# Optimization experiments

Measured on AMD Instinct MI355X. Metric: run time of the kernel, lower is better.

The kernel has to match this reference:

```python
import jax, jax.numpy as jnp
import numpy as np

N_NODES = 8192
N_EDGES = 524288
D_IN = 256
D_OUT = 256


def setup_inputs() -> dict:
    key = jax.random.key(0)
    ks = jax.random.split(key, 8)
    h = jax.random.normal(ks[0], (N_NODES, D_IN), dtype=jnp.float32)
    # Xavier-uniform-like scale for weights
    s = (6.0 / (D_IN + D_OUT)) ** 0.5
    W = jax.random.uniform(ks[1], (D_IN, D_OUT), jnp.float32, -s, s)
    Wq = jax.random.uniform(ks[2], (D_IN, D_OUT), jnp.float32, -s, s)
    bq = jnp.zeros((D_OUT,), jnp.float32)
    Wk = jax.random.uniform(ks[3], (D_IN, D_OUT), jnp.float32, -s, s)
    bk = jnp.zeros((D_OUT,), jnp.float32)
    senders = jax.random.randint(ks[4], (N_EDGES,), 0, N_NODES, dtype=jnp.int64 if jax.config.jax_enable_x64 else jnp.int32)
    receivers = jax.random.randint(ks[5], (N_EDGES,), 0, N_NODES, dtype=jnp.int64 if jax.config.jax_enable_x64 else jnp.int32)
    return {"h": h, "W": W, "Wq": Wq, "bq": bq, "Wk": Wk, "bk": bk,
            "senders": senders, "receivers": receivers}


def reference(h, W, Wq, bq, Wk, bk, senders, receivers):
    # Projected node features: (N, D_OUT)
    h_proj = jnp.dot(h, W)
    # Dense attention logits a = q @ k^T: (N, N), as in the original module
    q = jnp.dot(h, Wq) + bq
    k = jnp.dot(h, Wk) + bk
    a = jnp.dot(q, k.T)
    # Gather per-edge messages and attention weights, weight, scatter-add
    messages = h_proj[senders] * a[senders, receivers][:, None]  # (E, D_OUT)
    aggregated = jax.ops.segment_sum(messages, receivers, num_segments=h.shape[0])
    return jax.nn.relu(aggregated)
```

## Files before the change

kernel.cpp:

```cpp
#include <hip/hip_runtime.h>
#include <stdint.h>

typedef unsigned short u16;
typedef unsigned int u32;
typedef short v8s __attribute__((ext_vector_type(8)));
typedef float v4f __attribute__((ext_vector_type(4)));

#define N_NODES 8192
#define N_EDGES 524288
#define DFEAT 256
#define PADC 160

static __device__ __forceinline__ float bflo(u32 u) { return __uint_as_float(u << 16); }
static __device__ __forceinline__ float bfhi(u32 u) { return __uint_as_float(u & 0xffff0000u); }
static __device__ __forceinline__ u16 f2bf(float f) {
    u32 u = __float_as_uint(f);
    return (u16)((u + 0x7fffu + ((u >> 16) & 1u)) >> 16);
}

__global__ void prep_small(const float* __restrict__ w0, const float* __restrict__ w1,
                           const float* __restrict__ w2, u16* __restrict__ wt,
                           int* __restrict__ cnt) {
    int b = blockIdx.x;
    if (b < 48) {
        __shared__ u16 t[64][65];
        int region = b >> 4, tile = b & 15;
        int k0 = (tile >> 2) * 64, n0 = (tile & 3) * 64;
        const float* w = (region == 0) ? w0 : ((region == 1) ? w1 : w2);
        int tx = threadIdx.x & 63, ty = threadIdx.x >> 6;
#pragma unroll
        for (int it = 0; it < 16; it++) {
            int row = it * 4 + ty;
            t[row][tx] = f2bf(w[(k0 + row) * 256 + n0 + tx]);
        }
        __syncthreads();
        u16* o = wt + region * 65536;
#pragma unroll
        for (int it = 0; it < 16; it++) {
            int row = it * 4 + ty;
            o[(n0 + row) * 256 + k0 + tx] = t[tx][row];
        }
    } else {
        int i = ((b - 48) * 256 + threadIdx.x) * 4;
        *(int4*)(cnt + i) = make_int4(0, 0, 0, 0);
    }
}

__global__ __launch_bounds__(256) void main_mid(
    const float* __restrict__ h, const u16* __restrict__ wt,
    const float* __restrict__ bq, const float* __restrict__ bk,
    const int* __restrict__ recv, const int* __restrict__ send,
    u16* __restrict__ hproj, u16* __restrict__ qbuf, u16* __restrict__ kbuf,
    int* __restrict__ cnt, u16* __restrict__ es) {
    int b = blockIdx.x;
    if (b < 2048) {
        int e = b * 256 + threadIdx.x;
        int r = recv[e];
        int s = send[e];
        int pos = atomicAdd(&cnt[r], 1);
        if (pos < PADC) es[r * PADC + pos] = (u16)s;
    } else {
        int g = b - 2048;
        int wave = threadIdx.x >> 6, lane = threadIdx.x & 63;
        int lm = lane & 15, lq = lane >> 4;
        int bx = g & 127, by = g >> 7;
        int m0 = bx * 64 + wave * 16;
        int region = by >> 2, n0b = (by & 3) * 64;
        const u16* wtr = wt + region * 65536;

        v4f acc[4];
#pragma unroll
        for (int nt = 0; nt < 4; nt++) acc[nt] = (v4f){0.f, 0.f, 0.f, 0.f};

        const float* arow = h + (m0 + lm) * 256 + lq * 8;
#pragma unroll
        for (int k0 = 0; k0 < 256; k0 += 32) {
            float4 f0 = *(const float4*)(arow + k0);
            float4 f1 = *(const float4*)(arow + k0 + 4);
            v8s a;
            a[0] = (short)f2bf(f0.x); a[1] = (short)f2bf(f0.y);
            a[2] = (short)f2bf(f0.z); a[3] = (short)f2bf(f0.w);
            a[4] = (short)f2bf(f1.x); a[5] = (short)f2bf(f1.y);
            a[6] = (short)f2bf(f1.z); a[7] = (short)f2bf(f1.w);
#pragma unroll
            for (int nt = 0; nt < 4; nt++) {
                v8s bb = *(const v8s*)(wtr + (n0b + nt * 16 + lm) * 256 + k0 + lq * 8);
                acc[nt] = __builtin_amdgcn_mfma_f32_16x16x32_bf16(a, bb, acc[nt], 0, 0, 0);
            }
        }
        u16* outp = (region == 0) ? hproj : ((region == 1) ? qbuf : kbuf);
        const float* bias = (region == 1) ? bq : ((region == 2) ? bk : nullptr);
#pragma unroll
        for (int nt = 0; nt < 4; nt++) {
            int nn = n0b + nt * 16 + lm;
            float bv = bias ? bias[nn] : 0.f;
#pragma unroll
            for (int i = 0; i < 4; i++) {
                int m = m0 + lq * 4 + i;
                outp[m * 256 + nn] = f2bf(acc[nt][i] + bv);
            }
        }
    }
}


#define DOT8(Q) (kr0 * bflo((Q).x) + kr1 * bfhi((Q).x)                        \
               + kr2 * bflo((Q).y) + kr3 * bfhi((Q).y)                        \
               + kr4 * bflo((Q).z) + kr5 * bfhi((Q).z)                        \
               + kr6 * bflo((Q).w) + kr7 * bfhi((Q).w))

#define AXPY(P, H) do {                                                       \
    a0 += (P) * bflo((H).x); a1 += (P) * bfhi((H).x);                         \
    a2 += (P) * bflo((H).y); a3 += (P) * bfhi((H).y);                         \
    a4 += (P) * bflo((H).z); a5 += (P) * bfhi((H).z);                         \
    a6 += (P) * bflo((H).w); a7 += (P) * bfhi((H).w);                         \
} while (0)

#define DOT_AGG1(SIDX) do {                                                   \
    int off_ = (int)(SIDX) * 256 + cb;                                        \
    uint4 qv_ = *(const uint4*)(qbuf + off_);                                 \
    uint4 hv_ = *(const uint4*)(hpb + off_);                                  \
    float p_ = DOT8(qv_);                                                     \
    p_ += __shfl_xor(p_, 1, 32);  p_ += __shfl_xor(p_, 2, 32);                \
    p_ += __shfl_xor(p_, 4, 32);  p_ += __shfl_xor(p_, 8, 32);                \
    p_ += __shfl_xor(p_, 16, 32);                                             \
    AXPY(p_, hv_);                                                            \
} while (0)

__global__ __launch_bounds__(256, 4) void edge_fused(
    const u16* __restrict__ qbuf, const u16* __restrict__ kbuf,
    const u16* __restrict__ hpb, const int* __restrict__ cnt,
    const u16* __restrict__ es, float* __restrict__ out) {
    int wave = threadIdx.x >> 6, lane = threadIdx.x & 63;
    int r = blockIdx.x * 4 + wave;
    int lh = lane & 31, half = lane >> 5;
    int cb = lh * 8;
    int n = min(cnt[r], PADC);
    int base = r * PADC;

    uint4 kv = *(const uint4*)(kbuf + r * 256 + cb);
    float kr0 = bflo(kv.x), kr1 = bfhi(kv.x), kr2 = bflo(kv.y), kr3 = bfhi(kv.y),
          kr4 = bflo(kv.z), kr5 = bfhi(kv.z), kr6 = bflo(kv.w), kr7 = bfhi(kv.w);

    float a0 = 0.f, a1 = 0.f, a2 = 0.f, a3 = 0.f,
          a4 = 0.f, a5 = 0.f, a6 = 0.f, a7 = 0.f;

    uint2 sp = *(const uint2*)(es + base + half * 4);
    for (int c0 = 0; c0 < n; c0 += 8) {
        int nx = c0 + 8;
        uint2 spn = sp;
        if (nx < n) spn = *(const uint2*)(es + base + nx + half * 4);

        if (nx <= n) {
            int s0 = (int)(sp.x & 0xffffu), s1 = (int)(sp.x >> 16);
            int s2 = (int)(sp.y & 0xffffu), s3 = (int)(sp.y >> 16);
            int o0 = s0 * 256 + cb, o1 = s1 * 256 + cb;
            int o2 = s2 * 256 + cb, o3 = s3 * 256 + cb;
            uint4 q0 = *(const uint4*)(qbuf + o0);
            uint4 q1 = *(const uint4*)(qbuf + o1);
            uint4 q2 = *(const uint4*)(qbuf + o2);
            uint4 q3 = *(const uint4*)(qbuf + o3);
            uint4 h0 = *(const uint4*)(hpb + o0);
            uint4 h1 = *(const uint4*)(hpb + o1);
            uint4 h2 = *(const uint4*)(hpb + o2);
            uint4 h3 = *(const uint4*)(hpb + o3);
            float p0 = DOT8(q0);
            float p1 = DOT8(q1);
            float p2 = DOT8(q2);
            float p3 = DOT8(q3);
            p0 += __shfl_xor(p0, 1, 32);  p1 += __shfl_xor(p1, 1, 32);
            p2 += __shfl_xor(p2, 1, 32);  p3 += __shfl_xor(p3, 1, 32);
            p0 += __shfl_xor(p0, 2, 32);  p1 += __shfl_xor(p1, 2, 32);
            p2 += __shfl_xor(p2, 2, 32);  p3 += __shfl_xor(p3, 2, 32);
            p0 += __shfl_xor(p0, 4, 32);  p1 += __shfl_xor(p1, 4, 32);
            p2 += __shfl_xor(p2, 4, 32);  p3 += __shfl_xor(p3, 4, 32);
            p0 += __shfl_xor(p0, 8, 32);  p1 += __shfl_xor(p1, 8, 32);
            p2 += __shfl_xor(p2, 8, 32);  p3 += __shfl_xor(p3, 8, 32);
            p0 += __shfl_xor(p0, 16, 32); p1 += __shfl_xor(p1, 16, 32);
            p2 += __shfl_xor(p2, 16, 32); p3 += __shfl_xor(p3, 16, 32);
            AXPY(p0, h0);
            AXPY(p1, h1);
            AXPY(p2, h2);
            AXPY(p3, h3);
        } else {
            int mrem = n - c0 - half * 4;
            if (mrem > 0) DOT_AGG1(sp.x & 0xffffu);
            if (mrem > 1) DOT_AGG1(sp.x >> 16);
            if (mrem > 2) DOT_AGG1(sp.y & 0xffffu);
            if (mrem > 3) DOT_AGG1(sp.y >> 16);
        }
        sp = spn;
    }

    a0 += __shfl_xor(a0, 32, 64); a1 += __shfl_xor(a1, 32, 64);
    a2 += __shfl_xor(a2, 32, 64); a3 += __shfl_xor(a3, 32, 64);
    a4 += __shfl_xor(a4, 32, 64); a5 += __shfl_xor(a5, 32, 64);
    a6 += __shfl_xor(a6, 32, 64); a7 += __shfl_xor(a7, 32, 64);

    if (half == 0) {
        float4 o0, o1;
        o0.x = fmaxf(a0, 0.f); o0.y = fmaxf(a1, 0.f);
        o0.z = fmaxf(a2, 0.f); o0.w = fmaxf(a3, 0.f);
        o1.x = fmaxf(a4, 0.f); o1.y = fmaxf(a5, 0.f);
        o1.z = fmaxf(a6, 0.f); o1.w = fmaxf(a7, 0.f);
        float* op = out + r * 256 + cb;
        *(float4*)op = o0;
        *(float4*)(op + 4) = o1;
    }
}

extern "C" void kernel_launch(void* const* d_in, const int* in_sizes, int n_in,
                              void* d_out, int out_size, void* d_ws, size_t ws_size,
                              hipStream_t stream) {
    const float* h  = (const float*)d_in[0];
    const float* W  = (const float*)d_in[1];
    const float* Wq = (const float*)d_in[2];
    const float* bq = (const float*)d_in[3];
    const float* Wk = (const float*)d_in[4];
    const float* bk = (const float*)d_in[5];
    const int* senders   = (const int*)d_in[6];
    const int* receivers = (const int*)d_in[7];
    float* out = (float*)d_out;

    char* ws = (char*)d_ws;
    u16* wt    = (u16*)ws;
    u16* hproj = (u16*)(ws + 393216);
    u16* qbuf  = hproj + N_NODES * DFEAT;
    u16* kbuf  = qbuf + N_NODES * DFEAT;
    int* cnt   = (int*)(kbuf + N_NODES * DFEAT);
    u16* es    = (u16*)(cnt + N_NODES);

    prep_small<<<56, 256, 0, stream>>>(W, Wq, Wk, wt, cnt);
    main_mid<<<3584, 256, 0, stream>>>(h, wt, bq, bk, receivers, senders,
                                       hproj, qbuf, kbuf, cnt, es);
    edge_fused<<<N_NODES / 4, 256, 0, stream>>>(qbuf, kbuf, hproj, cnt, es, out);
}
```

Before: 182.2 us.

## Fuse all stages into one cooperative persistent kernel with grid syncs

Merges the weight transpose, edge bucketing, projection GEMMs and the edge aggregation into a single cooperative kernel. Grid-wide syncs separate the phases and blocks loop persistently over the work items, which removes two kernel launches and their gaps. It also pads the per-receiver counters to a 16-int stride to spread atomic contention, and widens the aggregation loop to 8 edges per half-wave for more loads in flight. In exchange it adds grid.sync costs and caps occupancy at what a cooperative launch can keep resident. The larger unrolled loop also raises register pressure.

```diff
diff --git a/kernel.cpp b/kernel.cpp
--- a/kernel.cpp
+++ b/kernel.cpp
@@ -1,5 +1,8 @@
 #include <hip/hip_runtime.h>
+#include <hip/hip_cooperative_groups.h>
 #include <stdint.h>
+
+namespace cg = cooperative_groups;
 
 typedef unsigned short u16;
 typedef unsigned int u32;
@@ -10,6 +13,7 @@
 #define N_EDGES 524288
 #define DFEAT 256
 #define PADC 160
+#define CNTS 16
 
 static __device__ __forceinline__ float bflo(u32 u) { return __uint_as_float(u << 16); }
 static __device__ __forceinline__ float bfhi(u32 u) { return __uint_as_float(u & 0xffff0000u); }
@@ -17,92 +21,6 @@
     u32 u = __float_as_uint(f);
     return (u16)((u + 0x7fffu + ((u >> 16) & 1u)) >> 16);
 }
-
-__global__ void prep_small(const float* __restrict__ w0, const float* __restrict__ w1,
-                           const float* __restrict__ w2, u16* __restrict__ wt,
-                           int* __restrict__ cnt) {
-    int b = blockIdx.x;
-    if (b < 48) {
-        __shared__ u16 t[64][65];
-        int region = b >> 4, tile = b & 15;
-        int k0 = (tile >> 2) * 64, n0 = (tile & 3) * 64;
-        const float* w = (region == 0) ? w0 : ((region == 1) ? w1 : w2);
-        int tx = threadIdx.x & 63, ty = threadIdx.x >> 6;
-#pragma unroll
-        for (int it = 0; it < 16; it++) {
-            int row = it * 4 + ty;
-            t[row][tx] = f2bf(w[(k0 + row) * 256 + n0 + tx]);
-        }
-        __syncthreads();
-        u16* o = wt + region * 65536;
-#pragma unroll
-        for (int it = 0; it < 16; it++) {
-            int row = it * 4 + ty;
-            o[(n0 + row) * 256 + k0 + tx] = t[tx][row];
-        }
-    } else {
-        int i = ((b - 48) * 256 + threadIdx.x) * 4;
-        *(int4*)(cnt + i) = make_int4(0, 0, 0, 0);
-    }
-}
-
-__global__ __launch_bounds__(256) void main_mid(
-    const float* __restrict__ h, const u16* __restrict__ wt,
-    const float* __restrict__ bq, const float* __restrict__ bk,
-    const int* __restrict__ recv, const int* __restrict__ send,
-    u16* __restrict__ hproj, u16* __restrict__ qbuf, u16* __restrict__ kbuf,
-    int* __restrict__ cnt, u16* __restrict__ es) {
-    int b = blockIdx.x;
-    if (b < 2048) {
-        int e = b * 256 + threadIdx.x;
-        int r = recv[e];
-        int s = send[e];
-        int pos = atomicAdd(&cnt[r], 1);
-        if (pos < PADC) es[r * PADC + pos] = (u16)s;
-    } else {
-        int g = b - 2048;
-        int wave = threadIdx.x >> 6, lane = threadIdx.x & 63;
-        int lm = lane & 15, lq = lane >> 4;
-        int bx = g & 127, by = g >> 7;
-        int m0 = bx * 64 + wave * 16;
-        int region = by >> 2, n0b = (by & 3) * 64;
-        const u16* wtr = wt + region * 65536;
-
-        v4f acc[4];
-#pragma unroll
-        for (int nt = 0; nt < 4; nt++) acc[nt] = (v4f){0.f, 0.f, 0.f, 0.f};
-
-        const float* arow = h + (m0 + lm) * 256 + lq * 8;
-#pragma unroll
-        for (int k0 = 0; k0 < 256; k0 += 32) {
-            float4 f0 = *(const float4*)(arow + k0);
-            float4 f1 = *(const float4*)(arow + k0 + 4);
-            v8s a;
-            a[0] = (short)f2bf(f0.x); a[1] = (short)f2bf(f0.y);
-            a[2] = (short)f2bf(f0.z); a[3] = (short)f2bf(f0.w);
-            a[4] = (short)f2bf(f1.x); a[5] = (short)f2bf(f1.y);
-            a[6] = (short)f2bf(f1.z); a[7] = (short)f2bf(f1.w);
-#pragma unroll
-            for (int nt = 0; nt < 4; nt++) {
-                v8s bb = *(const v8s*)(wtr + (n0b + nt * 16 + lm) * 256 + k0 + lq * 8);
-                acc[nt] = __builtin_amdgcn_mfma_f32_16x16x32_bf16(a, bb, acc[nt], 0, 0, 0);
-            }
-        }
-        u16* outp = (region == 0) ? hproj : ((region == 1) ? qbuf : kbuf);
-        const float* bias = (region == 1) ? bq : ((region == 2) ? bk : nullptr);
-#pragma unroll
-        for (int nt = 0; nt < 4; nt++) {
-            int nn = n0b + nt * 16 + lm;
-            float bv = bias ? bias[nn] : 0.f;
-#pragma unroll
-            for (int i = 0; i < 4; i++) {
-                int m = m0 + lq * 4 + i;
-                outp[m * 256 + nn] = f2bf(acc[nt][i] + bv);
-            }
-        }
-    }
-}
-
 
 #define DOT8(Q) (kr0 * bflo((Q).x) + kr1 * bfhi((Q).x)                        \
                + kr2 * bflo((Q).y) + kr3 * bfhi((Q).y)                        \
@@ -127,85 +45,182 @@
     AXPY(p_, hv_);                                                            \
 } while (0)
 
-__global__ __launch_bounds__(256, 4) void edge_fused(
-    const u16* __restrict__ qbuf, const u16* __restrict__ kbuf,
-    const u16* __restrict__ hpb, const int* __restrict__ cnt,
-    const u16* __restrict__ es, float* __restrict__ out) {
-    int wave = threadIdx.x >> 6, lane = threadIdx.x & 63;
-    int r = blockIdx.x * 4 + wave;
-    int lh = lane & 31, half = lane >> 5;
-    int cb = lh * 8;
-    int n = min(cnt[r], PADC);
-    int base = r * PADC;
-
-    uint4 kv = *(const uint4*)(kbuf + r * 256 + cb);
-    float kr0 = bflo(kv.x), kr1 = bfhi(kv.x), kr2 = bflo(kv.y), kr3 = bfhi(kv.y),
-          kr4 = bflo(kv.z), kr5 = bfhi(kv.z), kr6 = bflo(kv.w), kr7 = bfhi(kv.w);
-
-    float a0 = 0.f, a1 = 0.f, a2 = 0.f, a3 = 0.f,
-          a4 = 0.f, a5 = 0.f, a6 = 0.f, a7 = 0.f;
-
-    uint2 sp = *(const uint2*)(es + base + half * 4);
-    for (int c0 = 0; c0 < n; c0 += 8) {
-        int nx = c0 + 8;
-        uint2 spn = sp;
-        if (nx < n) spn = *(const uint2*)(es + base + nx + half * 4);
-
-        if (nx <= n) {
-            int s0 = (int)(sp.x & 0xffffu), s1 = (int)(sp.x >> 16);
-            int s2 = (int)(sp.y & 0xffffu), s3 = (int)(sp.y >> 16);
-            int o0 = s0 * 256 + cb, o1 = s1 * 256 + cb;
-            int o2 = s2 * 256 + cb, o3 = s3 * 256 + cb;
-            uint4 q0 = *(const uint4*)(qbuf + o0);
-            uint4 q1 = *(const uint4*)(qbuf + o1);
-            uint4 q2 = *(const uint4*)(qbuf + o2);
-            uint4 q3 = *(const uint4*)(qbuf + o3);
-            uint4 h0 = *(const uint4*)(hpb + o0);
-            uint4 h1 = *(const uint4*)(hpb + o1);
-            uint4 h2 = *(const uint4*)(hpb + o2);
-            uint4 h3 = *(const uint4*)(hpb + o3);
-            float p0 = DOT8(q0);
-            float p1 = DOT8(q1);
-            float p2 = DOT8(q2);
-            float p3 = DOT8(q3);
-            p0 += __shfl_xor(p0, 1, 32);  p1 += __shfl_xor(p1, 1, 32);
-            p2 += __shfl_xor(p2, 1, 32);  p3 += __shfl_xor(p3, 1, 32);
-            p0 += __shfl_xor(p0, 2, 32);  p1 += __shfl_xor(p1, 2, 32);
-            p2 += __shfl_xor(p2, 2, 32);  p3 += __shfl_xor(p3, 2, 32);
-            p0 += __shfl_xor(p0, 4, 32);  p1 += __shfl_xor(p1, 4, 32);
-            p2 += __shfl_xor(p2, 4, 32);  p3 += __shfl_xor(p3, 4, 32);
-            p0 += __shfl_xor(p0, 8, 32);  p1 += __shfl_xor(p1, 8, 32);
-            p2 += __shfl_xor(p2, 8, 32);  p3 += __shfl_xor(p3, 8, 32);
-            p0 += __shfl_xor(p0, 16, 32); p1 += __shfl_xor(p1, 16, 32);
-            p2 += __shfl_xor(p2, 16, 32); p3 += __shfl_xor(p3, 16, 32);
-            AXPY(p0, h0);
-            AXPY(p1, h1);
-            AXPY(p2, h2);
-            AXPY(p3, h3);
-        } else {
-            int mrem = n - c0 - half * 4;
-            if (mrem > 0) DOT_AGG1(sp.x & 0xffffu);
-            if (mrem > 1) DOT_AGG1(sp.x >> 16);
-            if (mrem > 2) DOT_AGG1(sp.y & 0xffffu);
-            if (mrem > 3) DOT_AGG1(sp.y >> 16);
-        }
-        sp = spn;
-    }
-
-    a0 += __shfl_xor(a0, 32, 64); a1 += __shfl_xor(a1, 32, 64);
-    a2 += __shfl_xor(a2, 32, 64); a3 += __shfl_xor(a3, 32, 64);
-    a4 += __shfl_xor(a4, 32, 64); a5 += __shfl_xor(a5, 32, 64);
-    a6 += __shfl_xor(a6, 32, 64); a7 += __shfl_xor(a7, 32, 64);
-
-    if (half == 0) {
-        float4 o0, o1;
-        o0.x = fmaxf(a0, 0.f); o0.y = fmaxf(a1, 0.f);
-        o0.z = fmaxf(a2, 0.f); o0.w = fmaxf(a3, 0.f);
-        o1.x = fmaxf(a4, 0.f); o1.y = fmaxf(a5, 0.f);
-        o1.z = fmaxf(a6, 0.f); o1.w = fmaxf(a7, 0.f);
-        float* op = out + r * 256 + cb;
-        *(float4*)op = o0;
-        *(float4*)(op + 4) = o1;
+#define LOADP(I, SIDX)                                                        \
+    int o##I = (int)(SIDX) * 256 + cb;                                        \
+    uint4 q##I = *(const uint4*)(qbuf + o##I);                                \
+    uint4 h##I = *(const uint4*)(hpb + o##I);
+
+__global__ __launch_bounds__(256, 4) void fused(
+    const float* __restrict__ h, const float* __restrict__ w0,
+    const float* __restrict__ w1, const float* __restrict__ w2,
+    const float* __restrict__ bq, const float* __restrict__ bk,
+    const int* __restrict__ recv, const int* __restrict__ send,
+    u16* __restrict__ wt, u16* __restrict__ hproj, u16* __restrict__ qbuf,
+    u16* __restrict__ kbuf, int* __restrict__ cnt, u16* __restrict__ es,
+    float* __restrict__ out)
+{
+    cg::grid_group grid = cg::this_grid();
+    const int nb = gridDim.x;
+    const int b = blockIdx.x;
+    const int tid = threadIdx.x;
+    const int wave = tid >> 6, lane = tid & 63;
+    __shared__ u16 t[64][65];
+
+    for (int i = b * 256 + tid; i < N_NODES * CNTS; i += nb * 256) cnt[i] = 0;
+
+    for (int j = b; j < 48; j += nb) {
+        int region = j >> 4, tile = j & 15;
+        int k0 = (tile >> 2) * 64, n0 = (tile & 3) * 64;
+        const float* w = (region == 0) ? w0 : ((region == 1) ? w1 : w2);
+        int tx = tid & 63, ty = tid >> 6;
+#pragma unroll
+        for (int it = 0; it < 16; it++) {
+            int row = it * 4 + ty;
+            t[row][tx] = f2bf(w[(k0 + row) * 256 + n0 + tx]);
+        }
+        __syncthreads();
+        u16* o = wt + region * 65536;
+#pragma unroll
+        for (int it = 0; it < 16; it++) {
+            int row = it * 4 + ty;
+            o[(n0 + row) * 256 + k0 + tx] = t[tx][row];
+        }
+        __syncthreads();
+    }
+
+    grid.sync();
+
+    for (int e = b * 256 + tid; e < N_EDGES; e += nb * 256) {
+        int r = recv[e];
+        int s = send[e];
+        int pos = atomicAdd(&cnt[r * CNTS], 1);
+        if (pos < PADC) es[r * PADC + pos] = (u16)s;
+    }
+
+    for (int j = b; j < 1536; j += nb) {
+        int lm = lane & 15, lq = lane >> 4;
+        int bx = j & 127, by = j >> 7;
+        int m0 = bx * 64 + wave * 16;
+        int region = by >> 2, n0b = (by & 3) * 64;
+        const u16* wtr = wt + region * 65536;
+
+        v4f acc[4];
+#pragma unroll
+        for (int nt = 0; nt < 4; nt++) acc[nt] = (v4f){0.f, 0.f, 0.f, 0.f};
+
+        const float* arow = h + (m0 + lm) * 256 + lq * 8;
+#pragma unroll
+        for (int k0 = 0; k0 < 256; k0 += 32) {
+            float4 f0 = *(const float4*)(arow + k0);
+            float4 f1 = *(const float4*)(arow + k0 + 4);
+            v8s a;
+            a[0] = (short)f2bf(f0.x); a[1] = (short)f2bf(f0.y);
+            a[2] = (short)f2bf(f0.z); a[3] = (short)f2bf(f0.w);
+            a[4] = (short)f2bf(f1.x); a[5] = (short)f2bf(f1.y);
+            a[6] = (short)f2bf(f1.z); a[7] = (short)f2bf(f1.w);
+#pragma unroll
+            for (int nt = 0; nt < 4; nt++) {
+                v8s bb = *(const v8s*)(wtr + (n0b + nt * 16 + lm) * 256 + k0 + lq * 8);
+                acc[nt] = __builtin_amdgcn_mfma_f32_16x16x32_bf16(a, bb, acc[nt], 0, 0, 0);
+            }
+        }
+        u16* outp = (region == 0) ? hproj : ((region == 1) ? qbuf : kbuf);
+        const float* bias = (region == 1) ? bq : ((region == 2) ? bk : nullptr);
+#pragma unroll
+        for (int nt = 0; nt < 4; nt++) {
+            int nn = n0b + nt * 16 + lm;
+            float bv = bias ? bias[nn] : 0.f;
+#pragma unroll
+            for (int i = 0; i < 4; i++) {
+                int m = m0 + lq * 4 + i;
+                outp[m * 256 + nn] = f2bf(acc[nt][i] + bv);
+            }
+        }
+    }
+
+    grid.sync();
+
+    const u16* hpb = hproj;
+    {
+        int lh = lane & 31, half = lane >> 5;
+        int cb = lh * 8;
+        for (int g = b; g < 2048; g += nb) {
+            int r = g * 4 + wave;
+            int n = min(cnt[r * CNTS], PADC);
+            int base = r * PADC;
+
+            uint4 kv = *(const uint4*)(kbuf + r * 256 + cb);
+            float kr0 = bflo(kv.x), kr1 = bfhi(kv.x), kr2 = bflo(kv.y), kr3 = bfhi(kv.y),
+                  kr4 = bflo(kv.z), kr5 = bfhi(kv.z), kr6 = bflo(kv.w), kr7 = bfhi(kv.w);
+
+            float a0 = 0.f, a1 = 0.f, a2 = 0.f, a3 = 0.f,
+                  a4 = 0.f, a5 = 0.f, a6 = 0.f, a7 = 0.f;
+
+            uint4 sp = *(const uint4*)(es + base + half * 8);
+            for (int c0 = 0; c0 < n; c0 += 16) {
+                int nx = c0 + 16;
+                uint4 spn = sp;
+                if (nx < n) spn = *(const uint4*)(es + base + nx + half * 8);
+
+                if (nx <= n) {
+                    LOADP(0, sp.x & 0xffffu) LOADP(1, sp.x >> 16)
+                    LOADP(2, sp.y & 0xffffu) LOADP(3, sp.y >> 16)
+                    LOADP(4, sp.z & 0xffffu) LOADP(5, sp.z >> 16)
+                    LOADP(6, sp.w & 0xffffu) LOADP(7, sp.w >> 16)
+                    float p0 = DOT8(q0), p1 = DOT8(q1), p2 = DOT8(q2), p3 = DOT8(q3);
+                    float p4 = DOT8(q4), p5 = DOT8(q5), p6 = DOT8(q6), p7 = DOT8(q7);
+                    p0 += __shfl_xor(p0, 1, 32);  p1 += __shfl_xor(p1, 1, 32);
+                    p2 += __shfl_xor(p2, 1, 32);  p3 += __shfl_xor(p3, 1, 32);
+                    p4 += __shfl_xor(p4, 1, 32);  p5 += __shfl_xor(p5, 1, 32);
+                    p6 += __shfl_xor(p6, 1, 32);  p7 += __shfl_xor(p7, 1, 32);
+                    p0 += __shfl_xor(p0, 2, 32);  p1 += __shfl_xor(p1, 2, 32);
+                    p2 += __shfl_xor(p2, 2, 32);  p3 += __shfl_xor(p3, 2, 32);
+                    p4 += __shfl_xor(p4, 2, 32);  p5 += __shfl_xor(p5, 2, 32);
+                    p6 += __shfl_xor(p6, 2, 32);  p7 += __shfl_xor(p7, 2, 32);
+                    p0 += __shfl_xor(p0, 4, 32);  p1 += __shfl_xor(p1, 4, 32);
+                    p2 += __shfl_xor(p2, 4, 32);  p3 += __shfl_xor(p3, 4, 32);
+                    p4 += __shfl_xor(p4, 4, 32);  p5 += __shfl_xor(p5, 4, 32);
+                    p6 += __shfl_xor(p6, 4, 32);  p7 += __shfl_xor(p7, 4, 32);
+                    p0 += __shfl_xor(p0, 8, 32);  p1 += __shfl_xor(p1, 8, 32);
+                    p2 += __shfl_xor(p2, 8, 32);  p3 += __shfl_xor(p3, 8, 32);
+                    p4 += __shfl_xor(p4, 8, 32);  p5 += __shfl_xor(p5, 8, 32);
+                    p6 += __shfl_xor(p6, 8, 32);  p7 += __shfl_xor(p7, 8, 32);
+                    p0 += __shfl_xor(p0, 16, 32); p1 += __shfl_xor(p1, 16, 32);
+                    p2 += __shfl_xor(p2, 16, 32); p3 += __shfl_xor(p3, 16, 32);
+                    p4 += __shfl_xor(p4, 16, 32); p5 += __shfl_xor(p5, 16, 32);
+                    p6 += __shfl_xor(p6, 16, 32); p7 += __shfl_xor(p7, 16, 32);
+                    AXPY(p0, h0); AXPY(p1, h1); AXPY(p2, h2); AXPY(p3, h3);
+                    AXPY(p4, h4); AXPY(p5, h5); AXPY(p6, h6); AXPY(p7, h7);
+                } else {
+                    int mrem = n - c0 - half * 8;
+                    if (mrem > 0) DOT_AGG1(sp.x & 0xffffu);
+                    if (mrem > 1) DOT_AGG1(sp.x >> 16);
+                    if (mrem > 2) DOT_AGG1(sp.y & 0xffffu);
+                    if (mrem > 3) DOT_AGG1(sp.y >> 16);
+                    if (mrem > 4) DOT_AGG1(sp.z & 0xffffu);
+                    if (mrem > 5) DOT_AGG1(sp.z >> 16);
+                    if (mrem > 6) DOT_AGG1(sp.w & 0xffffu);
+                    if (mrem > 7) DOT_AGG1(sp.w >> 16);
+                }
+                sp = spn;
+            }
+
+            a0 += __shfl_xor(a0, 32, 64); a1 += __shfl_xor(a1, 32, 64);
+            a2 += __shfl_xor(a2, 32, 64); a3 += __shfl_xor(a3, 32, 64);
+            a4 += __shfl_xor(a4, 32, 64); a5 += __shfl_xor(a5, 32, 64);
+            a6 += __shfl_xor(a6, 32, 64); a7 += __shfl_xor(a7, 32, 64);
+
+            if (half == 0) {
+                float4 o0, o1;
+                o0.x = fmaxf(a0, 0.f); o0.y = fmaxf(a1, 0.f);
+                o0.z = fmaxf(a2, 0.f); o0.w = fmaxf(a3, 0.f);
+                o1.x = fmaxf(a4, 0.f); o1.y = fmaxf(a5, 0.f);
+                o1.z = fmaxf(a6, 0.f); o1.w = fmaxf(a7, 0.f);
+                float* op = out + r * 256 + cb;
+                *(float4*)op = o0;
+                *(float4*)(op + 4) = o1;
+            }
+        }
     }
 }
 
@@ -228,10 +243,22 @@
     u16* qbuf  = hproj + N_NODES * DFEAT;
     u16* kbuf  = qbuf + N_NODES * DFEAT;
     int* cnt   = (int*)(kbuf + N_NODES * DFEAT);
-    u16* es    = (u16*)(cnt + N_NODES);
-
-    prep_small<<<56, 256, 0, stream>>>(W, Wq, Wk, wt, cnt);
-    main_mid<<<3584, 256, 0, stream>>>(h, wt, bq, bk, receivers, senders,
-                                       hproj, qbuf, kbuf, cnt, es);
-    edge_fused<<<N_NODES / 4, 256, 0, stream>>>(qbuf, kbuf, hproj, cnt, es, out);
+    u16* es    = (u16*)(cnt + N_NODES * CNTS);
+
+    static int nblk = 0;
+    if (nblk == 0) {
+        int bpc = 0;
+        if (hipOccupancyMaxActiveBlocksPerMultiprocessor(&bpc, fused, 256, 0) != hipSuccess
+            || bpc <= 0) bpc = 3;
+        nblk = bpc * 256;
+        if (nblk > 2048) nblk = 2048;
+    }
+
+    void* args[] = {
+        (void*)&h, (void*)&W, (void*)&Wq, (void*)&Wk, (void*)&bq, (void*)&bk,
+        (void*)&receivers, (void*)&senders,
+        (void*)&wt, (void*)&hproj, (void*)&qbuf, (void*)&kbuf,
+        (void*)&cnt, (void*)&es, (void*)&out
+    };
+    hipLaunchCooperativeKernel((void*)fused, dim3(nblk), dim3(256), args, 0, stream);
 }
```

New measurement: 312.6 us. +71.6%, slower.

## Software-pipeline edge gathers with double buffering and pad per-node counters

Applied to the files above, without the earlier changes.

The edge aggregation loop becomes a two-stage software pipeline. The next group of q/hproj rows is gathered while the dot products and AXPYs of the current group run, and the tail is handled once after the loop. Separately, each per-node atomic counter is padded to a 64-byte stride (CNTS=16) to cut contention and false sharing between neighbouring counters, which enlarges the zeroing launch in prep_small. The double buffering raises register pressure under the launch bound of 4 blocks, and the padded counters use more workspace.

```diff
diff --git a/kernel.cpp b/kernel.cpp
--- a/kernel.cpp
+++ b/kernel.cpp
@@ -10,6 +10,7 @@
 #define N_EDGES 524288
 #define DFEAT 256
 #define PADC 160
+#define CNTS 16
 
 static __device__ __forceinline__ float bflo(u32 u) { return __uint_as_float(u << 16); }
 static __device__ __forceinline__ float bfhi(u32 u) { return __uint_as_float(u & 0xffff0000u); }
@@ -57,7 +58,7 @@
         int e = b * 256 + threadIdx.x;
         int r = recv[e];
         int s = send[e];
-        int pos = atomicAdd(&cnt[r], 1);
+        int pos = atomicAdd(&cnt[r * CNTS], 1);
         if (pos < PADC) es[r * PADC + pos] = (u16)s;
     } else {
         int g = b - 2048;
@@ -127,6 +128,45 @@
     AXPY(p_, hv_);                                                            \
 } while (0)
 
+#define LOAD4(P, SP) do {                                                     \
+    int s0_ = (int)((SP).x & 0xffffu), s1_ = (int)((SP).x >> 16);             \
+    int s2_ = (int)((SP).y & 0xffffu), s3_ = (int)((SP).y >> 16);             \
+    q##P##0 = *(const uint4*)(qbuf + s0_ * 256 + cb);                         \
+    h##P##0 = *(const uint4*)(hpb  + s0_ * 256 + cb);                         \
+    q##P##1 = *(const uint4*)(qbuf + s1_ * 256 + cb);                         \
+    h##P##1 = *(const uint4*)(hpb  + s1_ * 256 + cb);                         \
+    q##P##2 = *(const uint4*)(qbuf + s2_ * 256 + cb);                         \
+    h##P##2 = *(const uint4*)(hpb  + s2_ * 256 + cb);                         \
+    q##P##3 = *(const uint4*)(qbuf + s3_ * 256 + cb);                         \
+    h##P##3 = *(const uint4*)(hpb  + s3_ * 256 + cb);                         \
+} while (0)
+
+#define COMP4(P) do {                                                         \
+    float p0_ = DOT8(q##P##0), p1_ = DOT8(q##P##1);                           \
+    float p2_ = DOT8(q##P##2), p3_ = DOT8(q##P##3);                           \
+    p0_ += __shfl_xor(p0_, 1, 32);  p1_ += __shfl_xor(p1_, 1, 32);            \
+    p2_ += __shfl_xor(p2_, 1, 32);  p3_ += __shfl_xor(p3_, 1, 32);            \
+    p0_ += __shfl_xor(p0_, 2, 32);  p1_ += __shfl_xor(p1_, 2, 32);            \
+    p2_ += __shfl_xor(p2_, 2, 32);  p3_ += __shfl_xor(p3_, 2, 32);            \
+    p0_ += __shfl_xor(p0_, 4, 32);  p1_ += __shfl_xor(p1_, 4, 32);            \
+    p2_ += __shfl_xor(p2_, 4, 32);  p3_ += __shfl_xor(p3_, 4, 32);            \
+    p0_ += __shfl_xor(p0_, 8, 32);  p1_ += __shfl_xor(p1_, 8, 32);            \
+    p2_ += __shfl_xor(p2_, 8, 32);  p3_ += __shfl_xor(p3_, 8, 32);            \
+    p0_ += __shfl_xor(p0_, 16, 32); p1_ += __shfl_xor(p1_, 16, 32);           \
+    p2_ += __shfl_xor(p2_, 16, 32); p3_ += __shfl_xor(p3_, 16, 32);           \
+    AXPY(p0_, h##P##0); AXPY(p1_, h##P##1);                                   \
+    AXPY(p2_, h##P##2); AXPY(p3_, h##P##3);                                   \
+} while (0)
+
+#define STAGE(CUR, NXT, TC) do {                                              \
+    if ((TC) + 1 < NT) {                                                      \
+        LOAD4(NXT, spn);                                                      \
+        if ((TC) + 2 < NT)                                                    \
+            spn = *(const uint2*)(es + base + ((TC) + 2) * 8 + half * 4);     \
+    }                                                                         \
+    COMP4(CUR);                                                               \
+} while (0)
+
 __global__ __launch_bounds__(256, 4) void edge_fused(
     const u16* __restrict__ qbuf, const u16* __restrict__ kbuf,
     const u16* __restrict__ hpb, const int* __restrict__ cnt,
@@ -135,7 +175,7 @@
     int r = blockIdx.x * 4 + wave;
     int lh = lane & 31, half = lane >> 5;
     int cb = lh * 8;
-    int n = min(cnt[r], PADC);
+    int n = min(cnt[r * CNTS], PADC);
     int base = r * PADC;
 
     uint4 kv = *(const uint4*)(kbuf + r * 256 + cb);
@@ -145,51 +185,28 @@
     float a0 = 0.f, a1 = 0.f, a2 = 0.f, a3 = 0.f,
           a4 = 0.f, a5 = 0.f, a6 = 0.f, a7 = 0.f;
 
-    uint2 sp = *(const uint2*)(es + base + half * 4);
-    for (int c0 = 0; c0 < n; c0 += 8) {
-        int nx = c0 + 8;
-        uint2 spn = sp;
-        if (nx < n) spn = *(const uint2*)(es + base + nx + half * 4);
-
-        if (nx <= n) {
-            int s0 = (int)(sp.x & 0xffffu), s1 = (int)(sp.x >> 16);
-            int s2 = (int)(sp.y & 0xffffu), s3 = (int)(sp.y >> 16);
-            int o0 = s0 * 256 + cb, o1 = s1 * 256 + cb;
-            int o2 = s2 * 256 + cb, o3 = s3 * 256 + cb;
-            uint4 q0 = *(const uint4*)(qbuf + o0);
-            uint4 q1 = *(const uint4*)(qbuf + o1);
-            uint4 q2 = *(const uint4*)(qbuf + o2);
-            uint4 q3 = *(const uint4*)(qbuf + o3);
-            uint4 h0 = *(const uint4*)(hpb + o0);
-            uint4 h1 = *(const uint4*)(hpb + o1);
-            uint4 h2 = *(const uint4*)(hpb + o2);
-            uint4 h3 = *(const uint4*)(hpb + o3);
-            float p0 = DOT8(q0);
-            float p1 = DOT8(q1);
-            float p2 = DOT8(q2);
-            float p3 = DOT8(q3);
-            p0 += __shfl_xor(p0, 1, 32);  p1 += __shfl_xor(p1, 1, 32);
-            p2 += __shfl_xor(p2, 1, 32);  p3 += __shfl_xor(p3, 1, 32);
-            p0 += __shfl_xor(p0, 2, 32);  p1 += __shfl_xor(p1, 2, 32);
-            p2 += __shfl_xor(p2, 2, 32);  p3 += __shfl_xor(p3, 2, 32);
-            p0 += __shfl_xor(p0, 4, 32);  p1 += __shfl_xor(p1, 4, 32);
-            p2 += __shfl_xor(p2, 4, 32);  p3 += __shfl_xor(p3, 4, 32);
-            p0 += __shfl_xor(p0, 8, 32);  p1 += __shfl_xor(p1, 8, 32);
-            p2 += __shfl_xor(p2, 8, 32);  p3 += __shfl_xor(p3, 8, 32);
-            p0 += __shfl_xor(p0, 16, 32); p1 += __shfl_xor(p1, 16, 32);
-            p2 += __shfl_xor(p2, 16, 32); p3 += __shfl_xor(p3, 16, 32);
-            AXPY(p0, h0);
-            AXPY(p1, h1);
-            AXPY(p2, h2);
-            AXPY(p3, h3);
-        } else {
-            int mrem = n - c0 - half * 4;
-            if (mrem > 0) DOT_AGG1(sp.x & 0xffffu);
-            if (mrem > 1) DOT_AGG1(sp.x >> 16);
-            if (mrem > 2) DOT_AGG1(sp.y & 0xffffu);
-            if (mrem > 3) DOT_AGG1(sp.y >> 16);
-        }
-        sp = spn;
+    int NT = n >> 3;
+    int m  = n & 7;
+
+    if (NT > 0) {
+        uint4 qc0, qc1, qc2, qc3, hc0, hc1, hc2, hc3;
+        uint4 qn0, qn1, qn2, qn3, hn0, hn1, hn2, hn3;
+        uint2 spc = *(const uint2*)(es + base + half * 4);
+        LOAD4(c, spc);
+        uint2 spn = spc;
+        if (NT > 1) spn = *(const uint2*)(es + base + 8 + half * 4);
+        for (int t = 0; t < NT; t += 2) {
+            STAGE(c, n, t);
+            if (t + 1 < NT) STAGE(n, c, t + 1);
+        }
+    }
+    if (m > 0) {
+        uint2 spT = *(const uint2*)(es + base + NT * 8 + half * 4);
+        int mrem = m - half * 4;
+        if (mrem > 0) DOT_AGG1(spT.x & 0xffffu);
+        if (mrem > 1) DOT_AGG1(spT.x >> 16);
+        if (mrem > 2) DOT_AGG1(spT.y & 0xffffu);
+        if (mrem > 3) DOT_AGG1(spT.y >> 16);
     }
 
     a0 += __shfl_xor(a0, 32, 64); a1 += __shfl_xor(a1, 32, 64);
@@ -228,9 +245,9 @@
     u16* qbuf  = hproj + N_NODES * DFEAT;
     u16* kbuf  = qbuf + N_NODES * DFEAT;
     int* cnt   = (int*)(kbuf + N_NODES * DFEAT);
-    u16* es    = (u16*)(cnt + N_NODES);
-
-    prep_small<<<56, 256, 0, stream>>>(W, Wq, Wk, wt, cnt);
+    u16* es    = (u16*)(cnt + N_NODES * CNTS);
+
+    prep_small<<<176, 256, 0, stream>>>(W, Wq, Wk, wt, cnt);
     main_mid<<<3584, 256, 0, stream>>>(h, wt, bq, bk, receivers, senders,
                                        hproj, qbuf, kbuf, cnt, es);
     edge_fused<<<N_NODES / 4, 256, 0, stream>>>(qbuf, kbuf, hproj, cnt, es, out);
```

After: 181.0 us. No clear change (-0.7%).
